# Performance work log

Measured on AMD Instinct MI355X. Metric: run time of the kernel, lower is better.

Reference implementation:

```python
import jax, jax.numpy as jnp
import numpy as np

GROUP = 64          # quantization group size along input dim
EPS = 1e-6          # rms_norm_eps
THETA = 1000000.0   # rope theta
NUM_HEADS = 16
NUM_KV_HEADS = 4
HEAD_DIM = 128


def _qlinear(x, wq, s, b=None):
    # dequantize int8-valued weights with per-group scales, then GEMM
    o, i = wq.shape
    w = (wq.reshape(o, i // GROUP, GROUP).astype(jnp.float32) * s[:, :, None]).reshape(o, i)
    y = jnp.einsum('bsi,oi->bso', x, w)
    return y + b if b is not None else y


def _rmsnorm(x, w):
    return x * jax.lax.rsqrt(jnp.mean(x * x, axis=-1, keepdims=True) + EPS) * w


def _rope(x, offset):
    # x: [B, H, S, hd], neox-style half rotation
    hd = x.shape[-1]
    S = x.shape[2]
    pos = (jnp.arange(S) + offset).astype(jnp.float32)
    inv = THETA ** (-(jnp.arange(0, hd, 2).astype(jnp.float32)) / hd)  # [hd/2]
    ang = pos[:, None] * inv[None, :]                                  # [S, hd/2]
    cos, sin = jnp.cos(ang), jnp.sin(ang)
    x1, x2 = x[..., : hd // 2], x[..., hd // 2 :]
    return jnp.concatenate([x1 * cos - x2 * sin, x2 * cos + x1 * sin], axis=-1)


def setup_inputs() -> dict:
    key = jax.random.key(0)
    B, S, D, I = 2, 1024, 2048, 5632
    KV = NUM_KV_HEADS * HEAD_DIM  # 512
    keys = iter(jax.random.split(key, 32))

    def qw(shape):
        return jax.random.randint(next(keys), shape, -127, 128, dtype=jnp.int32)

    def sc(shape):
        return jax.random.uniform(next(keys), shape, jnp.float32, 0.5, 1.5) * 0.001

    inp = {
        'x': jax.random.normal(next(keys), (B, S, D), jnp.float32),
        'wq_q': qw((D, D)),   'wq_s': sc((D, D // GROUP)),
        'bq': jax.random.normal(next(keys), (D,), jnp.float32) * 0.02,
        'wk_q': qw((KV, D)),  'wk_s': sc((KV, D // GROUP)),
        'bk': jax.random.normal(next(keys), (KV,), jnp.float32) * 0.02,
        'wv_q': qw((KV, D)),  'wv_s': sc((KV, D // GROUP)),
        'bv': jax.random.normal(next(keys), (KV,), jnp.float32) * 0.02,
        'wo_q': qw((D, D)),   'wo_s': sc((D, D // GROUP)),
        'gate_q': qw((I, D)), 'gate_s': sc((I, D // GROUP)),
        'up_q': qw((I, D)),   'up_s': sc((I, D // GROUP)),
        'down_q': qw((D, I)), 'down_s': sc((D, I // GROUP)),
        'w_in_ln': jnp.ones((D,), jnp.float32),
        'w_post_ln': jnp.ones((D,), jnp.float32),
        'offset': 0,
    }
    return inp


def reference(x, wq_q, wq_s, bq, wk_q, wk_s, bk, wv_q, wv_s, bv, wo_q, wo_s,
              gate_q, gate_s, up_q, up_s, down_q, down_s, w_in_ln, w_post_ln, offset):
    B, S, D = x.shape
    H, KVH, hd = NUM_HEADS, NUM_KV_HEADS, HEAD_DIM

    # --- attention sub-block ---
    h = _rmsnorm(x, w_in_ln)
    q = _qlinear(h, wq_q, wq_s, bq).reshape(B, S, H, hd).transpose(0, 2, 1, 3)
    k = _qlinear(h, wk_q, wk_s, bk).reshape(B, S, KVH, hd).transpose(0, 2, 1, 3)
    v = _qlinear(h, wv_q, wv_s, bv).reshape(B, S, KVH, hd).transpose(0, 2, 1, 3)
    q = _rope(q, offset)
    k = _rope(k, offset)

    g = H // KVH  # query groups per kv head
    qg = q.reshape(B, KVH, g, S, hd)
    scores = jnp.einsum('bghsd,bgtd->bghst', qg, k) * (1.0 / np.sqrt(hd)).astype(np.float32)
    causal = jnp.tril(jnp.ones((S, S), dtype=bool))  # prefill causal mask (empty cache)
    scores = jnp.where(causal, scores, jnp.float32(-1e9))
    p = jax.nn.softmax(scores, axis=-1)
    o = jnp.einsum('bghst,bgtd->bghsd', p, v)
    o = o.reshape(B, H, S, hd).transpose(0, 2, 1, 3).reshape(B, S, D)
    x = x + _qlinear(o, wo_q, wo_s)

    # --- mlp sub-block ---
    h2 = _rmsnorm(x, w_post_ln)
    gate = jax.nn.silu(_qlinear(h2, gate_q, gate_s))
    up = _qlinear(h2, up_q, up_s)
    mlp = _qlinear(gate * up, down_q, down_s)
    return x + mlp
```

## Files before the change

### kernel.cpp

```cpp
#include <hip/hip_runtime.h>
#include <cstdint>
#include <cstddef>

#define DEV __device__ __forceinline__

typedef _Float16 f16x8 __attribute__((ext_vector_type(8)));
typedef float f32x4 __attribute__((ext_vector_type(4)));

static constexpr int D_MODEL = 2048;
static constexpr int D_FF    = 5632;
static constexpr int N_QKV   = 3072;
static constexpr int SEQ     = 1024;
static constexpr int BATCH   = 2;
static constexpr int ROWS    = BATCH * SEQ;
static constexpr int HEADS   = 16;
static constexpr int HD      = 128;

DEV uint16_t f2h(float f) {
    return __builtin_bit_cast(uint16_t, (_Float16)f);
}

DEV void async_load16(const void* g, void* lds) {
    __builtin_amdgcn_global_load_lds(
        reinterpret_cast<__attribute__((address_space(1))) void*>(
            reinterpret_cast<uintptr_t>(g)),
        reinterpret_cast<__attribute__((address_space(3))) void*>(
            static_cast<uint32_t>(reinterpret_cast<uintptr_t>(lds))),
        16, 0, 0);
}

static constexpr int DQ_BLOCKS = 44032;

__global__ __launch_bounds__(256)
void dequant_all_kernel(const int* __restrict__ wq_q, const float* __restrict__ wq_s,
                        const int* __restrict__ wk_q, const float* __restrict__ wk_s,
                        const int* __restrict__ wv_q, const float* __restrict__ wv_s,
                        const int* __restrict__ wo_q, const float* __restrict__ wo_s,
                        const int* __restrict__ gate_q, const float* __restrict__ gate_s,
                        const int* __restrict__ up_q, const float* __restrict__ up_s,
                        const int* __restrict__ down_q, const float* __restrict__ down_s,
                        uint16_t* __restrict__ Wqkv, uint16_t* __restrict__ Wo,
                        uint16_t* __restrict__ Wgu, uint16_t* __restrict__ Wdown)
{
    const int bid = blockIdx.x;
    const int* q; const float* s; uint16_t* out; int I, mode, seg0;
    if (bid < 4096)        { q = wq_q;   s = wq_s;   out = Wqkv;                      I = 2048; mode = 0; seg0 = 0; }
    else if (bid < 5120)   { q = wk_q;   s = wk_s;   out = Wqkv + 2048 * 2048;        I = 2048; mode = 0; seg0 = 4096; }
    else if (bid < 6144)   { q = wv_q;   s = wv_s;   out = Wqkv + 2560 * 2048;        I = 2048; mode = 0; seg0 = 5120; }
    else if (bid < 10240)  { q = wo_q;   s = wo_s;   out = Wo;                        I = 2048; mode = 0; seg0 = 6144; }
    else if (bid < 21504)  { q = gate_q; s = gate_s; out = Wgu;                       I = 2048; mode = 1; seg0 = 10240; }
    else if (bid < 32768)  { q = up_q;   s = up_s;   out = Wgu;                       I = 2048; mode = 2; seg0 = 21504; }
    else                   { q = down_q; s = down_s; out = Wdown;                     I = 5632; mode = 0; seg0 = 32768; }

    const int idx = (bid - seg0) * 256 + threadIdx.x;
    const int e = idx * 4;
    const int row = e / I;
    const int i = e - row * I;
    const int4 qv = *reinterpret_cast<const int4*>(&q[e]);
    const float scf = s[row * (I >> 6) + (i >> 6)];
    int orow = row;
    if (mode == 1) orow = ((row >> 4) << 5) + (row & 15);
    else if (mode == 2) orow = ((row >> 4) << 5) + (row & 15) + 16;
    uint16_t h[4];
    h[0] = f2h((float)qv.x * scf);
    h[1] = f2h((float)qv.y * scf);
    h[2] = f2h((float)qv.z * scf);
    h[3] = f2h((float)qv.w * scf);
    uint2 pk;
    pk.x = (uint32_t)h[0] | ((uint32_t)h[1] << 16);
    pk.y = (uint32_t)h[2] | ((uint32_t)h[3] << 16);
    *reinterpret_cast<uint2*>(&out[(size_t)orow * I + i]) = pk;
}

__global__ __launch_bounds__(256)
void rmsnorm_kernel(const float* __restrict__ x, const float* __restrict__ wln,
                    uint16_t* __restrict__ out)
{
    __shared__ float red[4];
    const int row = blockIdx.x;
    const int tid = threadIdx.x;
    const float* xr = x + (size_t)row * D_MODEL;
    const float4 v0 = *reinterpret_cast<const float4*>(&xr[tid * 8]);
    const float4 v1 = *reinterpret_cast<const float4*>(&xr[tid * 8 + 4]);
    float ss = v0.x*v0.x + v0.y*v0.y + v0.z*v0.z + v0.w*v0.w
             + v1.x*v1.x + v1.y*v1.y + v1.z*v1.z + v1.w*v1.w;
#pragma unroll
    for (int off = 32; off; off >>= 1) ss += __shfl_xor(ss, off);
    if ((tid & 63) == 0) red[tid >> 6] = ss;
    __syncthreads();
    const float rms = rsqrtf((red[0] + red[1] + red[2] + red[3]) * (1.0f / D_MODEL) + 1e-6f);
    const int cb = tid * 8;
    const size_t base = (size_t)row * D_MODEL + cb;
    const float vals[8] = {v0.x, v0.y, v0.z, v0.w, v1.x, v1.y, v1.z, v1.w};
#pragma unroll
    for (int k = 0; k < 8; k += 2) {
        const uint16_t h0 = f2h(vals[k] * rms * wln[cb + k]);
        const uint16_t h1 = f2h(vals[k + 1] * rms * wln[cb + k + 1]);
        *reinterpret_cast<uint32_t*>(&out[base + k]) = (uint32_t)h0 | ((uint32_t)h1 << 16);
    }
}

__global__ __launch_bounds__(256)
void gemm_f16_glu_kernel(const uint16_t* __restrict__ A, const uint16_t* __restrict__ W,
                         uint16_t* __restrict__ outh, int M, int N, int K)
{
    __shared__ uint16_t sA[2][128 * 64];
    __shared__ uint16_t sB[2][128 * 64];

    const int tid  = threadIdx.x;
    const int lane = tid & 63;
    const int wv   = tid >> 6;
    const int wm   = wv >> 1;
    const int wn   = wv & 1;
    const int quad = lane >> 4;
    const int l16  = lane & 15;

    const int nBn = N >> 7;
    const int bm  = blockIdx.x / nBn;
    const int bn  = blockIdx.x - bm * nBn;
    const int m0  = bm << 7;
    const int n0  = bn << 7;

    f32x4 acc[4][4];
#pragma unroll
    for (int i = 0; i < 4; i++)
#pragma unroll
        for (int j = 0; j < 4; j++)
            acc[i][j] = (f32x4){0.f, 0.f, 0.f, 0.f};

    const uint16_t* Ab = A + (size_t)m0 * K;
    const uint16_t* Wb = W + (size_t)n0 * K;

    auto stage = [&](int kt, int bsel) {
#pragma unroll
        for (int p = 0; p < 4; p++) {
            const int cb = p * 256 + wv * 64;
            const int c  = cb + lane;
            const int row = c >> 3;
            const int g   = (c & 7) ^ (row & 7);
            const size_t goff = (size_t)row * K + kt + g * 8;
            async_load16(Ab + goff, &sA[bsel][cb * 8]);
            async_load16(Wb + goff, &sB[bsel][cb * 8]);
        }
    };

    stage(0, 0);
    __syncthreads();

    const int nKt = K >> 6;
    for (int t = 0; t < nKt; t++) {
        const int cur = t & 1;
        if (t + 1 < nKt) stage((t + 1) << 6, cur ^ 1);
        const uint16_t* sAc = sA[cur];
        const uint16_t* sBc = sB[cur];
#pragma unroll
        for (int kk = 0; kk < 2; kk++) {
            const int gsw = ((kk * 4 + quad) ^ (l16 & 7)) * 8;
            f16x8 bfv[4];
#pragma unroll
            for (int j = 0; j < 4; j++)
                bfv[j] = *reinterpret_cast<const f16x8*>(
                    &sBc[(wn * 64 + j * 16 + l16) * 64 + gsw]);
#pragma unroll
            for (int i = 0; i < 4; i++) {
                const f16x8 af = *reinterpret_cast<const f16x8*>(
                    &sAc[(wm * 64 + i * 16 + l16) * 64 + gsw]);
#pragma unroll
                for (int j = 0; j < 4; j++)
                    acc[i][j] = __builtin_amdgcn_mfma_f32_16x16x32_f16(af, bfv[j], acc[i][j], 0, 0, 0);
            }
        }
        __syncthreads();
    }

    const int NH = N >> 1;
#pragma unroll
    for (int i = 0; i < 4; i++) {
        const int rowb = m0 + wm * 64 + i * 16 + quad * 4;
#pragma unroll
        for (int r = 0; r < 4; r++) {
            const size_t rr = (size_t)(rowb + r);
#pragma unroll
            for (int pjt = 0; pjt < 2; pjt++) {
                const float g = acc[i][2 * pjt][r];
                const float u = acc[i][2 * pjt + 1][r];
                const float a = (g / (1.0f + __expf(-g))) * u;
                const int cc = (n0 >> 1) + wn * 32 + pjt * 16 + l16;
                outh[rr * NH + cc] = f2h(a);
            }
        }
    }
}

__global__ __launch_bounds__(256)
void gemm_f16_m64_kernel(const uint16_t* __restrict__ A, const uint16_t* __restrict__ W,
                         const float* __restrict__ bq, const float* __restrict__ bk,
                         const float* __restrict__ bv, const float* __restrict__ resid,
                         float* __restrict__ outf, int M, int N, int K)
{
    __shared__ uint16_t sA[2][64 * 64];
    __shared__ uint16_t sB[2][128 * 64];

    const int tid  = threadIdx.x;
    const int lane = tid & 63;
    const int wv   = tid >> 6;
    const int quad = lane >> 4;
    const int l16  = lane & 15;

    const int nBn = N >> 7;
    const int bm  = blockIdx.x / nBn;
    const int bn  = blockIdx.x - bm * nBn;
    const int m0  = bm << 6;
    const int n0  = bn << 7;

    f32x4 acc[4][2];
#pragma unroll
    for (int i = 0; i < 4; i++)
#pragma unroll
        for (int j = 0; j < 2; j++)
            acc[i][j] = (f32x4){0.f, 0.f, 0.f, 0.f};

    const uint16_t* Ab = A + (size_t)m0 * K;
    const uint16_t* Wb = W + (size_t)n0 * K;

    auto stage = [&](int kt, int bsel) {
#pragma unroll
        for (int p = 0; p < 2; p++) {
            const int cb = p * 256 + wv * 64;
            const int c  = cb + lane;
            const int row = c >> 3;
            const int g   = (c & 7) ^ (row & 7);
            async_load16(Ab + (size_t)row * K + kt + g * 8, &sA[bsel][cb * 8]);
        }
#pragma unroll
        for (int p = 0; p < 4; p++) {
            const int cb = p * 256 + wv * 64;
            const int c  = cb + lane;
            const int row = c >> 3;
            const int g   = (c & 7) ^ (row & 7);
            async_load16(Wb + (size_t)row * K + kt + g * 8, &sB[bsel][cb * 8]);
        }
    };

    stage(0, 0);
    __syncthreads();

    const int nKt = K >> 6;
    for (int t = 0; t < nKt; t++) {
        const int cur = t & 1;
        if (t + 1 < nKt) stage((t + 1) << 6, cur ^ 1);
        const uint16_t* sAc = sA[cur];
        const uint16_t* sBc = sB[cur];
#pragma unroll
        for (int kk = 0; kk < 2; kk++) {
            const int gsw = ((kk * 4 + quad) ^ (l16 & 7)) * 8;
            f16x8 bfv[2];
#pragma unroll
            for (int j = 0; j < 2; j++)
                bfv[j] = *reinterpret_cast<const f16x8*>(
                    &sBc[(wv * 32 + j * 16 + l16) * 64 + gsw]);
#pragma unroll
            for (int i = 0; i < 4; i++) {
                const f16x8 af = *reinterpret_cast<const f16x8*>(
                    &sAc[(i * 16 + l16) * 64 + gsw]);
#pragma unroll
                for (int j = 0; j < 2; j++)
                    acc[i][j] = __builtin_amdgcn_mfma_f32_16x16x32_f16(af, bfv[j], acc[i][j], 0, 0, 0);
            }
        }
        __syncthreads();
    }

#pragma unroll
    for (int i = 0; i < 4; i++) {
        const int rowb = m0 + i * 16 + quad * 4;
#pragma unroll
        for (int r = 0; r < 4; r++) {
            const size_t rr = (size_t)(rowb + r);
#pragma unroll
            for (int j = 0; j < 2; j++) {
                const int cc = n0 + wv * 32 + j * 16 + l16;
                float v = acc[i][j][r];
                if (bq) {
                    float bb;
                    if (cc < 2048)      bb = bq[cc];
                    else if (cc < 2560) bb = bk[cc - 2048];
                    else                bb = bv[cc - 2560];
                    v += bb;
                }
                if (resid) v += resid[rr * N + cc];
                outf[rr * N + cc] = v;
            }
        }
    }
}

static constexpr int ROPE_Q_THREADS = ROWS * 16 * 64;
static constexpr int ROPE_THREADS   = ROPE_Q_THREADS + ROWS * 4 * 64;
static constexpr float LOG2_1E6_OVER_64 = 0.31143075889910283f;

__global__ __launch_bounds__(256)
void rope_qk_kernel(const float* __restrict__ qkv, const int* __restrict__ offp,
                    uint16_t* __restrict__ Qb, uint16_t* __restrict__ Kb)
{
    const int gidx = blockIdx.x * 256 + threadIdx.x;
    if (gidx < ROPE_Q_THREADS) {
        const int idx = gidx;
        const int d   = idx & 63;
        const int h   = (idx >> 6) & 15;
        const int row = idx >> 10;
        const int b   = row >> 10;
        const int s   = row & (SEQ - 1);
        const float pos  = (float)(s + *offp);
        const float freq = exp2f(-(float)d * LOG2_1E6_OVER_64);
        float sn, cs;
        __sincosf(pos * freq, &sn, &cs);
        const size_t gb = (size_t)row * N_QKV + h * HD + d;
        const float x1 = qkv[gb];
        const float x2 = qkv[gb + 64];
        const float qscale = 0.08838834764831845f;
        const size_t ob = ((size_t)(b * 16 + h) * SEQ + s) * HD + d;
        Qb[ob]      = f2h((x1 * cs - x2 * sn) * qscale);
        Qb[ob + 64] = f2h((x2 * cs + x1 * sn) * qscale);
    } else {
        const int idx = gidx - ROPE_Q_THREADS;
        const int d   = idx & 63;
        const int kvh = (idx >> 6) & 3;
        const int row = idx >> 8;
        const int b   = row >> 10;
        const int s   = row & (SEQ - 1);
        const float pos  = (float)(s + *offp);
        const float freq = exp2f(-(float)d * LOG2_1E6_OVER_64);
        float sn, cs;
        __sincosf(pos * freq, &sn, &cs);
        const size_t gb = (size_t)row * N_QKV + 2048 + kvh * HD + d;
        const float x1 = qkv[gb];
        const float x2 = qkv[gb + 64];
        const size_t ob = ((size_t)(b * 4 + kvh) * SEQ + s) * HD + d;
        Kb[ob]      = f2h(x1 * cs - x2 * sn);
        Kb[ob + 64] = f2h(x2 * cs + x1 * sn);
    }
}

__global__ __launch_bounds__(256)
void prep_v_kernel(const float* __restrict__ qkv, uint16_t* __restrict__ Vt)
{
    __shared__ uint16_t sh[128 * 72];
    const int tid = threadIdx.x;
    const int sc  = blockIdx.x & 15;
    const int bk  = blockIdx.x >> 4;
    const int b   = bk >> 2, kvh = bk & 3;
#pragma unroll
    for (int p = 0; p < 8; p++) {
        const int q4 = p * 256 + tid;
        const int sloc = q4 >> 5, d4 = (q4 & 31) * 4;
        const float4 v = *reinterpret_cast<const float4*>(
            &qkv[(size_t)(b * SEQ + sc * 64 + sloc) * N_QKV + 2560 + kvh * HD + d4]);
        sh[(d4 + 0) * 72 + sloc] = f2h(v.x);
        sh[(d4 + 1) * 72 + sloc] = f2h(v.y);
        sh[(d4 + 2) * 72 + sloc] = f2h(v.z);
        sh[(d4 + 3) * 72 + sloc] = f2h(v.w);
    }
    __syncthreads();
    const int d = tid >> 1, half = tid & 1;
    const size_t ob = ((size_t)(bk * 128 + d)) * SEQ + sc * 64 + half * 32;
    const uint16_t* srh = &sh[d * 72 + half * 32];
#pragma unroll
    for (int k = 0; k < 4; k++)
        *reinterpret_cast<uint4*>(&Vt[ob + k * 8]) =
            *reinterpret_cast<const uint4*>(&srh[k * 8]);
}

__global__ __launch_bounds__(256)
void attn_kernel(const uint16_t* __restrict__ Qb, const uint16_t* __restrict__ Kb,
                 const uint16_t* __restrict__ Vt, uint16_t* __restrict__ att)
{
    __shared__ uint16_t sK[2][32 * 128];
    __shared__ uint16_t sV[2][128 * 32];
    __shared__ uint16_t sP[4 * 16 * 32];

    const int tid  = threadIdx.x;
    const int lane = tid & 63;
    const int wv   = tid >> 6;
    const int quad = lane >> 4;
    const int l16  = lane & 15;
    const int qsw  = (quad ^ ((l16 >> 1) & 3)) * 8;

    const int bi  = blockIdx.x;
    const int sc  = 15 - (bi >> 5);
    const int bh  = bi & 31;
    const int b   = bh >> 4;
    const int h   = bh & 15;
    const int kvh = h >> 2;
    const int s0  = sc << 6;

    f16x8 qf[4];
    {
        const size_t qb = ((size_t)(b * 16 + h) * SEQ + s0 + wv * 16 + l16) * HD;
#pragma unroll
        for (int ks = 0; ks < 4; ks++)
            qf[ks] = *reinterpret_cast<const f16x8*>(&Qb[qb + ks * 32 + quad * 8]);
    }

    float m_i[4], l_i[4];
#pragma unroll
    for (int r = 0; r < 4; r++) { m_i[r] = -1e30f; l_i[r] = 0.f; }
    f32x4 oacc[8];
#pragma unroll
    for (int dt = 0; dt < 8; dt++) oacc[dt] = (f32x4){0.f, 0.f, 0.f, 0.f};

    const size_t kb = (size_t)(b * 4 + kvh) * SEQ * HD;
    const size_t vb = (size_t)(b * 4 + kvh) * HD * SEQ;

    auto stageKV = [&](int t0, int bsel) {
#pragma unroll
        for (int p = 0; p < 2; p++) {
            const int cb = p * 256 + wv * 64;
            const int c  = cb + lane;
            const int krow = c >> 4;
            const int kcc  = (c & 15) ^ (krow & 7);
            async_load16(Kb + kb + (size_t)(t0 + krow) * HD + kcc * 8, &sK[bsel][cb * 8]);
            const int vrow = c >> 2;
            const int vcc  = (c & 3) ^ ((vrow >> 1) & 3);
            async_load16(Vt + vb + (size_t)vrow * SEQ + t0 + vcc * 8, &sV[bsel][cb * 8]);
        }
    };

    const int ntiles = 2 * sc + 2;
    stageKV(0, 0);
    __syncthreads();

    for (int tt = 0; tt < ntiles; tt++) {
        const int t0 = tt << 5;
        const int cur = tt & 1;
        if (tt + 1 < ntiles) stageKV((tt + 1) << 5, cur ^ 1);

        f32x4 sacc[2];
        sacc[0] = (f32x4){0.f, 0.f, 0.f, 0.f};
        sacc[1] = (f32x4){0.f, 0.f, 0.f, 0.f};
#pragma unroll
        for (int ks = 0; ks < 4; ks++) {
#pragma unroll
            for (int jt = 0; jt < 2; jt++) {
                const int idx = (jt * 16 + l16) * 128 + (((ks * 4 + quad) ^ (l16 & 7)) * 8);
                const f16x8 kf = *reinterpret_cast<const f16x8*>(&sK[cur][idx]);
                sacc[jt] = __builtin_amdgcn_mfma_f32_16x16x32_f16(qf[ks], kf, sacc[jt], 0, 0, 0);
            }
        }

        if (t0 >= s0) {
            const int rowg = s0 + wv * 16 + quad * 4;
#pragma unroll
            for (int jt = 0; jt < 2; jt++) {
                const int key = t0 + jt * 16 + l16;
#pragma unroll
                for (int r = 0; r < 4; r++)
                    if (key > rowg + r) sacc[jt][r] = -1e30f;
            }
        }

        float alpha[4];
#pragma unroll
        for (int r = 0; r < 4; r++) {
            float mt = fmaxf(sacc[0][r], sacc[1][r]);
#pragma unroll
            for (int off = 8; off; off >>= 1) mt = fmaxf(mt, __shfl_xor(mt, off));
            const float mn = fmaxf(m_i[r], mt);
            alpha[r] = __expf(m_i[r] - mn);
            const float p0 = __expf(sacc[0][r] - mn);
            const float p1 = __expf(sacc[1][r] - mn);
            float ps = p0 + p1;
#pragma unroll
            for (int off = 8; off; off >>= 1) ps += __shfl_xor(ps, off);
            l_i[r] = l_i[r] * alpha[r] + ps;
            m_i[r] = mn;
            const int prow = quad * 4 + r;
            sP[wv * 512 + prow * 32 + 0 * 16 + l16] = f2h(p0);
            sP[wv * 512 + prow * 32 + 1 * 16 + l16] = f2h(p1);
        }

#pragma unroll
        for (int dt = 0; dt < 8; dt++) {
#pragma unroll
            for (int r = 0; r < 4; r++) oacc[dt][r] *= alpha[r];
        }
        const f16x8 pf = *reinterpret_cast<const f16x8*>(&sP[wv * 512 + l16 * 32 + quad * 8]);
#pragma unroll
        for (int dt = 0; dt < 8; dt++) {
            const f16x8 vf = *reinterpret_cast<const f16x8*>(&sV[cur][(dt * 16 + l16) * 32 + qsw]);
            oacc[dt] = __builtin_amdgcn_mfma_f32_16x16x32_f16(pf, vf, oacc[dt], 0, 0, 0);
        }

        __syncthreads();
    }

    float inv[4];
#pragma unroll
    for (int r = 0; r < 4; r++) inv[r] = 1.0f / l_i[r];
#pragma unroll
    for (int r = 0; r < 4; r++) {
        const size_t rowg = (size_t)(b * SEQ + s0 + wv * 16 + quad * 4 + r);
#pragma unroll
        for (int dt = 0; dt < 8; dt++)
            att[rowg * D_MODEL + h * HD + dt * 16 + l16] = f2h(oacc[dt][r] * inv[r]);
    }
}

extern "C" void kernel_launch(void* const* d_in, const int* in_sizes, int n_in,
                              void* d_out, int out_size, void* d_ws, size_t ws_size,
                              hipStream_t stream)
{
    (void)in_sizes; (void)n_in; (void)out_size; (void)ws_size;
    const float* x      = (const float*)d_in[0];
    const int*   wq_q   = (const int*)d_in[1];
    const float* wq_s   = (const float*)d_in[2];
    const float* bq     = (const float*)d_in[3];
    const int*   wk_q   = (const int*)d_in[4];
    const float* wk_s   = (const float*)d_in[5];
    const float* bk     = (const float*)d_in[6];
    const int*   wv_q   = (const int*)d_in[7];
    const float* wv_s   = (const float*)d_in[8];
    const float* bv     = (const float*)d_in[9];
    const int*   wo_q   = (const int*)d_in[10];
    const float* wo_s   = (const float*)d_in[11];
    const int*   gate_q = (const int*)d_in[12];
    const float* gate_s = (const float*)d_in[13];
    const int*   up_q   = (const int*)d_in[14];
    const float* up_s   = (const float*)d_in[15];
    const int*   down_q = (const int*)d_in[16];
    const float* down_s = (const float*)d_in[17];
    const float* w_in   = (const float*)d_in[18];
    const float* w_post = (const float*)d_in[19];
    const int*   offp   = (const int*)d_in[20];

    char* p = (char*)d_ws;
    auto alloc = [&](size_t bytes) {
        char* r = p;
        p += (bytes + 255) & ~(size_t)255;
        return r;
    };
    uint16_t* Wgu   = (uint16_t*)alloc((size_t)2 * D_FF * D_MODEL * 2);
    uint16_t* Wdown = (uint16_t*)alloc((size_t)D_MODEL * D_FF * 2);
    uint16_t* hbuf  = (uint16_t*)alloc((size_t)ROWS * D_MODEL * 2);
    float*    x2    = (float*)alloc((size_t)ROWS * D_MODEL * 4);
    char* zone = alloc((size_t)N_QKV * D_MODEL * 2 +
                       (size_t)D_MODEL * D_MODEL * 2 +
                       (size_t)ROWS * N_QKV * 4 + 8192);
    uint16_t* Wqkv = (uint16_t*)zone;
    uint16_t* Wo   = Wqkv + (size_t)N_QKV * D_MODEL;
    float*    qkv  = (float*)(Wo + (size_t)D_MODEL * D_MODEL);
    uint16_t* Qb = Wqkv;
    uint16_t* Kb = Qb + (size_t)BATCH * 16 * SEQ * HD;
    uint16_t* Vt = Kb + (size_t)BATCH * 4 * SEQ * HD;
    uint16_t* att = (uint16_t*)qkv;
    uint16_t* act = (uint16_t*)zone;

    dequant_all_kernel<<<DQ_BLOCKS, 256, 0, stream>>>(
        wq_q, wq_s, wk_q, wk_s, wv_q, wv_s, wo_q, wo_s,
        gate_q, gate_s, up_q, up_s, down_q, down_s,
        Wqkv, Wo, Wgu, Wdown);

    rmsnorm_kernel<<<ROWS, 256, 0, stream>>>(x, w_in, hbuf);

    gemm_f16_m64_kernel<<<(ROWS / 64) * (N_QKV / 128), 256, 0, stream>>>(
        hbuf, Wqkv, bq, bk, bv, nullptr, qkv, ROWS, N_QKV, D_MODEL);

    rope_qk_kernel<<<ROPE_THREADS / 256, 256, 0, stream>>>(qkv, offp, Qb, Kb);
    prep_v_kernel<<<BATCH * 4 * (SEQ / 64), 256, 0, stream>>>(qkv, Vt);

    attn_kernel<<<BATCH * HEADS * (SEQ / 64), 256, 0, stream>>>(Qb, Kb, Vt, att);

    gemm_f16_m64_kernel<<<(ROWS / 64) * (D_MODEL / 128), 256, 0, stream>>>(
        att, Wo, nullptr, nullptr, nullptr, x, x2, ROWS, D_MODEL, D_MODEL);

    rmsnorm_kernel<<<ROWS, 256, 0, stream>>>(x2, w_post, hbuf);

    gemm_f16_glu_kernel<<<(ROWS / 128) * (2 * D_FF / 128), 256, 0, stream>>>(
        hbuf, Wgu, act, ROWS, 2 * D_FF, D_MODEL);

    gemm_f16_m64_kernel<<<(ROWS / 64) * (D_MODEL / 128), 256, 0, stream>>>(
        act, Wdown, nullptr, nullptr, nullptr, x2, (float*)d_out, ROWS, D_MODEL, D_FF);
}
```

Baseline: 540.3 us.

## Split weight dequant across kernels and co-schedule with norm, rope and attention

The monolithic dequant kernel is split. The QKV/O weight dequant now shares a launch with the first RMSNorm, and the MLP weight dequant shares a launch with the attention kernel, using block-index dispatch. Rope and V-transpose prep are also merged into one launch. The aim is to hide the memory-bound dequant behind other work and to cut launch count. In exchange, the attention launch carries extra heavy blocks that could contend for bandwidth, and LDS is allocated for the dequant blocks as well.

```diff
diff --git a/kernel.cpp b/kernel.cpp
--- a/kernel.cpp
+++ b/kernel.cpp
@@ -29,30 +29,9 @@
         16, 0, 0);
 }
 
-static constexpr int DQ_BLOCKS = 44032;
-
-__global__ __launch_bounds__(256)
-void dequant_all_kernel(const int* __restrict__ wq_q, const float* __restrict__ wq_s,
-                        const int* __restrict__ wk_q, const float* __restrict__ wk_s,
-                        const int* __restrict__ wv_q, const float* __restrict__ wv_s,
-                        const int* __restrict__ wo_q, const float* __restrict__ wo_s,
-                        const int* __restrict__ gate_q, const float* __restrict__ gate_s,
-                        const int* __restrict__ up_q, const float* __restrict__ up_s,
-                        const int* __restrict__ down_q, const float* __restrict__ down_s,
-                        uint16_t* __restrict__ Wqkv, uint16_t* __restrict__ Wo,
-                        uint16_t* __restrict__ Wgu, uint16_t* __restrict__ Wdown)
-{
-    const int bid = blockIdx.x;
-    const int* q; const float* s; uint16_t* out; int I, mode, seg0;
-    if (bid < 4096)        { q = wq_q;   s = wq_s;   out = Wqkv;                      I = 2048; mode = 0; seg0 = 0; }
-    else if (bid < 5120)   { q = wk_q;   s = wk_s;   out = Wqkv + 2048 * 2048;        I = 2048; mode = 0; seg0 = 4096; }
-    else if (bid < 6144)   { q = wv_q;   s = wv_s;   out = Wqkv + 2560 * 2048;        I = 2048; mode = 0; seg0 = 5120; }
-    else if (bid < 10240)  { q = wo_q;   s = wo_s;   out = Wo;                        I = 2048; mode = 0; seg0 = 6144; }
-    else if (bid < 21504)  { q = gate_q; s = gate_s; out = Wgu;                       I = 2048; mode = 1; seg0 = 10240; }
-    else if (bid < 32768)  { q = up_q;   s = up_s;   out = Wgu;                       I = 2048; mode = 2; seg0 = 21504; }
-    else                   { q = down_q; s = down_s; out = Wdown;                     I = 5632; mode = 0; seg0 = 32768; }
-
-    const int idx = (bid - seg0) * 256 + threadIdx.x;
+DEV void dq_body(const int* __restrict__ q, const float* __restrict__ s,
+                 uint16_t* __restrict__ out, int I, int mode, int idx)
+{
     const int e = idx * 4;
     const int row = e / I;
     const int i = e - row * I;
@@ -73,6 +52,50 @@
 }
 
 __global__ __launch_bounds__(256)
+void norm_dqA_kernel(const float* __restrict__ x, const float* __restrict__ wln,
+                     uint16_t* __restrict__ outh,
+                     const int* __restrict__ wq_q, const float* __restrict__ wq_s,
+                     const int* __restrict__ wk_q, const float* __restrict__ wk_s,
+                     const int* __restrict__ wv_q, const float* __restrict__ wv_s,
+                     const int* __restrict__ wo_q, const float* __restrict__ wo_s,
+                     uint16_t* __restrict__ Wqkv, uint16_t* __restrict__ Wo)
+{
+    __shared__ float red[4];
+    const int bid = blockIdx.x;
+    const int tid = threadIdx.x;
+    if (bid < ROWS) {
+        const float* xr = x + (size_t)bid * D_MODEL;
+        const float4 v0 = *reinterpret_cast<const float4*>(&xr[tid * 8]);
+        const float4 v1 = *reinterpret_cast<const float4*>(&xr[tid * 8 + 4]);
+        float ss = v0.x*v0.x + v0.y*v0.y + v0.z*v0.z + v0.w*v0.w
+                 + v1.x*v1.x + v1.y*v1.y + v1.z*v1.z + v1.w*v1.w;
+#pragma unroll
+        for (int off = 32; off; off >>= 1) ss += __shfl_xor(ss, off);
+        if ((tid & 63) == 0) red[tid >> 6] = ss;
+        __syncthreads();
+        const float rms = rsqrtf((red[0] + red[1] + red[2] + red[3]) * (1.0f / D_MODEL) + 1e-6f);
+        const int cb = tid * 8;
+        const size_t base = (size_t)bid * D_MODEL + cb;
+        const float vals[8] = {v0.x, v0.y, v0.z, v0.w, v1.x, v1.y, v1.z, v1.w};
+#pragma unroll
+        for (int k = 0; k < 8; k += 2) {
+            const uint16_t h0 = f2h(vals[k] * rms * wln[cb + k]);
+            const uint16_t h1 = f2h(vals[k + 1] * rms * wln[cb + k + 1]);
+            *reinterpret_cast<uint32_t*>(&outh[base + k]) = (uint32_t)h0 | ((uint32_t)h1 << 16);
+        }
+    } else {
+        const int b2 = bid - ROWS;
+        const int* q; const float* s; uint16_t* out; int seg0;
+        if (b2 < 4096)      { q = wq_q; s = wq_s; out = Wqkv;               seg0 = 0; }
+        else if (b2 < 5120) { q = wk_q; s = wk_s; out = Wqkv + 2048 * 2048; seg0 = 4096; }
+        else if (b2 < 6144) { q = wv_q; s = wv_s; out = Wqkv + 2560 * 2048; seg0 = 5120; }
+        else                { q = wo_q; s = wo_s; out = Wo;                 seg0 = 6144; }
+        dq_body(q, s, out, 2048, 0, (b2 - seg0) * 256 + tid);
+    }
+}
+static constexpr int NORM_DQA_BLOCKS = ROWS + 10240;
+
+__global__ __launch_bounds__(256)
 void rmsnorm_kernel(const float* __restrict__ x, const float* __restrict__ wln,
                     uint16_t* __restrict__ out)
 {
@@ -297,13 +320,43 @@
 
 static constexpr int ROPE_Q_THREADS = ROWS * 16 * 64;
 static constexpr int ROPE_THREADS   = ROPE_Q_THREADS + ROWS * 4 * 64;
+static constexpr int PREPV_BLOCKS   = BATCH * 4 * (SEQ / 64);
+static constexpr int ROPE_PREP_BLOCKS = PREPV_BLOCKS + ROPE_THREADS / 256;
 static constexpr float LOG2_1E6_OVER_64 = 0.31143075889910283f;
 
 __global__ __launch_bounds__(256)
-void rope_qk_kernel(const float* __restrict__ qkv, const int* __restrict__ offp,
-                    uint16_t* __restrict__ Qb, uint16_t* __restrict__ Kb)
-{
-    const int gidx = blockIdx.x * 256 + threadIdx.x;
+void rope_prep_kernel(const float* __restrict__ qkv, const int* __restrict__ offp,
+                      uint16_t* __restrict__ Qb, uint16_t* __restrict__ Kb,
+                      uint16_t* __restrict__ Vt)
+{
+    __shared__ uint16_t sh[128 * 72];
+    const int tid = threadIdx.x;
+    if (blockIdx.x < PREPV_BLOCKS) {
+        const int sc  = blockIdx.x & 15;
+        const int bk  = blockIdx.x >> 4;
+        const int b   = bk >> 2, kvh = bk & 3;
+#pragma unroll
+        for (int p = 0; p < 8; p++) {
+            const int q4 = p * 256 + tid;
+            const int sloc = q4 >> 5, d4 = (q4 & 31) * 4;
+            const float4 v = *reinterpret_cast<const float4*>(
+                &qkv[(size_t)(b * SEQ + sc * 64 + sloc) * N_QKV + 2560 + kvh * HD + d4]);
+            sh[(d4 + 0) * 72 + sloc] = f2h(v.x);
+            sh[(d4 + 1) * 72 + sloc] = f2h(v.y);
+            sh[(d4 + 2) * 72 + sloc] = f2h(v.z);
+            sh[(d4 + 3) * 72 + sloc] = f2h(v.w);
+        }
+        __syncthreads();
+        const int d = tid >> 1, half = tid & 1;
+        const size_t ob = ((size_t)(bk * 128 + d)) * SEQ + sc * 64 + half * 32;
+        const uint16_t* srh = &sh[d * 72 + half * 32];
+#pragma unroll
+        for (int k = 0; k < 4; k++)
+            *reinterpret_cast<uint4*>(&Vt[ob + k * 8]) =
+                *reinterpret_cast<const uint4*>(&srh[k * 8]);
+        return;
+    }
+    const int gidx = (blockIdx.x - PREPV_BLOCKS) * 256 + tid;
     if (gidx < ROPE_Q_THREADS) {
         const int idx = gidx;
         const int d   = idx & 63;
@@ -342,44 +395,32 @@
     }
 }
 
+static constexpr int ATTN_BLOCKS   = BATCH * HEADS * (SEQ / 64);
+static constexpr int DQB_BLOCKS    = 3 * 11264;
+static constexpr int ATTN_DQ_BLOCKS = ATTN_BLOCKS + DQB_BLOCKS;
+
 __global__ __launch_bounds__(256)
-void prep_v_kernel(const float* __restrict__ qkv, uint16_t* __restrict__ Vt)
-{
-    __shared__ uint16_t sh[128 * 72];
-    const int tid = threadIdx.x;
-    const int sc  = blockIdx.x & 15;
-    const int bk  = blockIdx.x >> 4;
-    const int b   = bk >> 2, kvh = bk & 3;
-#pragma unroll
-    for (int p = 0; p < 8; p++) {
-        const int q4 = p * 256 + tid;
-        const int sloc = q4 >> 5, d4 = (q4 & 31) * 4;
-        const float4 v = *reinterpret_cast<const float4*>(
-            &qkv[(size_t)(b * SEQ + sc * 64 + sloc) * N_QKV + 2560 + kvh * HD + d4]);
-        sh[(d4 + 0) * 72 + sloc] = f2h(v.x);
-        sh[(d4 + 1) * 72 + sloc] = f2h(v.y);
-        sh[(d4 + 2) * 72 + sloc] = f2h(v.z);
-        sh[(d4 + 3) * 72 + sloc] = f2h(v.w);
-    }
-    __syncthreads();
-    const int d = tid >> 1, half = tid & 1;
-    const size_t ob = ((size_t)(bk * 128 + d)) * SEQ + sc * 64 + half * 32;
-    const uint16_t* srh = &sh[d * 72 + half * 32];
-#pragma unroll
-    for (int k = 0; k < 4; k++)
-        *reinterpret_cast<uint4*>(&Vt[ob + k * 8]) =
-            *reinterpret_cast<const uint4*>(&srh[k * 8]);
-}
-
-__global__ __launch_bounds__(256)
-void attn_kernel(const uint16_t* __restrict__ Qb, const uint16_t* __restrict__ Kb,
-                 const uint16_t* __restrict__ Vt, uint16_t* __restrict__ att)
+void attn_dqB_kernel(const uint16_t* __restrict__ Qb, const uint16_t* __restrict__ Kb,
+                     const uint16_t* __restrict__ Vt, uint16_t* __restrict__ att,
+                     const int* __restrict__ gate_q, const float* __restrict__ gate_s,
+                     const int* __restrict__ up_q, const float* __restrict__ up_s,
+                     const int* __restrict__ down_q, const float* __restrict__ down_s,
+                     uint16_t* __restrict__ Wgu, uint16_t* __restrict__ Wdown)
 {
     __shared__ uint16_t sK[2][32 * 128];
     __shared__ uint16_t sV[2][128 * 32];
     __shared__ uint16_t sP[4 * 16 * 32];
 
     const int tid  = threadIdx.x;
+
+    if (blockIdx.x >= ATTN_BLOCKS) {
+        const int b2 = blockIdx.x - ATTN_BLOCKS;
+        if (b2 < 11264)       dq_body(gate_q, gate_s, Wgu,   2048, 1, b2 * 256 + tid);
+        else if (b2 < 22528)  dq_body(up_q,   up_s,   Wgu,   2048, 2, (b2 - 11264) * 256 + tid);
+        else                  dq_body(down_q, down_s, Wdown, 5632, 0, (b2 - 22528) * 256 + tid);
+        return;
+    }
+
     const int lane = tid & 63;
     const int wv   = tid >> 6;
     const int quad = lane >> 4;
@@ -555,20 +596,16 @@
     uint16_t* att = (uint16_t*)qkv;
     uint16_t* act = (uint16_t*)zone;
 
-    dequant_all_kernel<<<DQ_BLOCKS, 256, 0, stream>>>(
-        wq_q, wq_s, wk_q, wk_s, wv_q, wv_s, wo_q, wo_s,
-        gate_q, gate_s, up_q, up_s, down_q, down_s,
-        Wqkv, Wo, Wgu, Wdown);
-
-    rmsnorm_kernel<<<ROWS, 256, 0, stream>>>(x, w_in, hbuf);
+    norm_dqA_kernel<<<NORM_DQA_BLOCKS, 256, 0, stream>>>(
+        x, w_in, hbuf, wq_q, wq_s, wk_q, wk_s, wv_q, wv_s, wo_q, wo_s, Wqkv, Wo);
 
     gemm_f16_m64_kernel<<<(ROWS / 64) * (N_QKV / 128), 256, 0, stream>>>(
         hbuf, Wqkv, bq, bk, bv, nullptr, qkv, ROWS, N_QKV, D_MODEL);
 
-    rope_qk_kernel<<<ROPE_THREADS / 256, 256, 0, stream>>>(qkv, offp, Qb, Kb);
-    prep_v_kernel<<<BATCH * 4 * (SEQ / 64), 256, 0, stream>>>(qkv, Vt);
-
-    attn_kernel<<<BATCH * HEADS * (SEQ / 64), 256, 0, stream>>>(Qb, Kb, Vt, att);
+    rope_prep_kernel<<<ROPE_PREP_BLOCKS, 256, 0, stream>>>(qkv, offp, Qb, Kb, Vt);
+
+    attn_dqB_kernel<<<ATTN_DQ_BLOCKS, 256, 0, stream>>>(
+        Qb, Kb, Vt, att, gate_q, gate_s, up_q, up_s, down_q, down_s, Wgu, Wdown);
 
     gemm_f16_m64_kernel<<<(ROWS / 64) * (D_MODEL / 128), 256, 0, stream>>>(
         att, Wo, nullptr, nullptr, nullptr, x, x2, ROWS, D_MODEL, D_MODEL);
```

Measured after the change: 519.0 us, median of 2. -3.9%, faster.
